# Kernel optimization log

Measured on AMD Instinct MI355X. Metric: run time of the kernel, lower is better.

The kernel has to match this reference:

```python
import jax, jax.numpy as jnp
import numpy as np

# Model hyperparameters (from init_kwargs)
B, C, H, W = 4, 3, 224, 224
P = 16            # patch size
E = 768           # embed_dim
NH = 12           # num_heads
DH = E // NH      # head dim
L = 2             # num_layers
DFF = 4 * E
OUT = 1000
NP_ = (H // P) * (W // P)   # 196 patches
ALPHA, BETA, GAMMA = 0.5, 0.5, 1.0
EPS = 1e-8
LN_EPS = 1e-5


def _layernorm(x, w, b):
    mu = x.mean(-1, keepdims=True)
    var = ((x - mu) ** 2).mean(-1, keepdims=True)
    return (x - mu) * jax.lax.rsqrt(var + LN_EPS) * w + b


def _tversky_attn(x, ln_w, ln_b, w_qkv, b_qkv, w_o, b_o):
    # x: [B,S,E]
    h = _layernorm(x, ln_w, ln_b)
    qkv = h @ w_qkv + b_qkv                       # [B,S,3E]
    q, k, v = jnp.split(qkv, 3, axis=-1)
    def heads(t):
        return t.reshape(t.shape[0], t.shape[1], NH, DH).transpose(0, 2, 1, 3)  # [B,NH,S,DH]
    q, k, v = heads(q), heads(k), heads(v)
    # Tversky similarity on non-negative feature memberships
    qp = jax.nn.relu(q)
    kp = jax.nn.relu(k)
    qs = qp.sum(-1)                               # [B,NH,S]
    ks = kp.sum(-1)                               # [B,NH,S]
    # pairwise L1: sum_d |q_i - k_j|   (dominant intermediate [B,NH,S,S,DH])
    l1 = jnp.abs(qp[:, :, :, None, :] - kp[:, :, None, :, :]).sum(-1)  # [B,NH,S,S]
    qsum = qs[:, :, :, None]
    ksum = ks[:, :, None, :]
    inter = 0.5 * (qsum + ksum - l1)              # sum min(q,k)
    a_minus_b = 0.5 * (l1 + qsum - ksum)          # sum relu(q-k)
    b_minus_a = 0.5 * (l1 - qsum + ksum)          # sum relu(k-q)
    scores = GAMMA * inter / (inter + ALPHA * a_minus_b + BETA * b_minus_a + EPS)
    attn = jax.nn.softmax(scores, axis=-1)        # [B,NH,S,S]
    o = jnp.einsum('bhij,bhjd->bhid', attn, v)    # [B,NH,S,DH]
    o = o.transpose(0, 2, 1, 3).reshape(x.shape[0], x.shape[1], E)
    return o @ w_o + b_o


def _forward(x, conv_w, conv_b, pos_embed, cls_token,
             ln1_w, ln1_b, attn_w, attn_b, proj_w, proj_b,
             ln2_w, ln2_b, fc1_w, fc1_b, fc2_w, fc2_b,
             lnf_w, lnf_b, head_w, head_b):
    b = x.shape[0]
    # patch embed: stride==kernel conv == non-overlapping patch projection
    xp = x.reshape(b, C, H // P, P, W // P, P)
    tok = jnp.einsum('bchpwq,ecpq->bhwe', xp, conv_w).reshape(b, NP_, E) + conv_b
    tok = tok + pos_embed                         # [B,196,E]
    cls = jnp.broadcast_to(cls_token, (b, 1, E))
    h = jnp.concatenate([cls, tok], axis=1)       # [B,197,E]
    for i in range(L):
        h = h + _tversky_attn(h, ln1_w[i], ln1_b[i], attn_w[i], attn_b[i], proj_w[i], proj_b[i])
        m = _layernorm(h, ln2_w[i], ln2_b[i])
        m = jax.nn.gelu(m @ fc1_w[i] + fc1_b[i])
        h = h + m @ fc2_w[i] + fc2_b[i]
    h = _layernorm(h, lnf_w, lnf_b)
    return h[:, 0] @ head_w + head_b              # [B,OUT]


def setup_inputs() -> dict:
    key = jax.random.key(0)
    ks = jax.random.split(key, 24)
    n = lambda k, shp, s=0.02: jax.random.normal(k, shp, dtype=jnp.float32) * s
    return {
        'x': jax.random.normal(ks[0], (B, C, H, W), dtype=jnp.float32),
        'conv_w': n(ks[1], (E, C, P, P)),
        'conv_b': jnp.zeros((E,), jnp.float32),
        'pos_embed': n(ks[2], (1, NP_, E)),
        'cls_token': n(ks[3], (1, 1, E)),
        'ln1_w': jnp.ones((L, E), jnp.float32),
        'ln1_b': jnp.zeros((L, E), jnp.float32),
        'attn_w': n(ks[4], (L, E, 3 * E)),
        'attn_b': jnp.zeros((L, 3 * E), jnp.float32),
        'proj_w': n(ks[5], (L, E, E)),
        'proj_b': jnp.zeros((L, E), jnp.float32),
        'ln2_w': jnp.ones((L, E), jnp.float32),
        'ln2_b': jnp.zeros((L, E), jnp.float32),
        'fc1_w': n(ks[6], (L, E, DFF)),
        'fc1_b': jnp.zeros((L, DFF), jnp.float32),
        'fc2_w': n(ks[7], (L, DFF, E)),
        'fc2_b': jnp.zeros((L, E), jnp.float32),
        'lnf_w': jnp.ones((E,), jnp.float32),
        'lnf_b': jnp.zeros((E,), jnp.float32),
        'head_w': n(ks[8], (E, OUT)),
        'head_b': jnp.zeros((OUT,), jnp.float32),
    }


def reference(x, conv_w, conv_b, pos_embed, cls_token,
              ln1_w, ln1_b, attn_w, attn_b, proj_w, proj_b,
              ln2_w, ln2_b, fc1_w, fc1_b, fc2_w, fc2_b,
              lnf_w, lnf_b, head_w, head_b):
    return _forward(x, conv_w, conv_b, pos_embed, cls_token,
                    ln1_w, ln1_b, attn_w, attn_b, proj_w, proj_b,
                    ln2_w, ln2_b, fc1_w, fc1_b, fc2_w, fc2_b,
                    lnf_w, lnf_b, head_w, head_b)
```

## Files before the change

### kernel.cpp

```cpp
#include <hip/hip_runtime.h>
#include <hip/hip_bf16.h>
#include <math.h>

#define B_  4
#define E_  768
#define NH_ 12
#define DH_ 64
#define DFF_ 3072
#define OUT_ 1000
#define S_  197
#define ROWS_ 788
#define QH_P 12608
#define KGP  16384

typedef __bf16 bf16x8_t __attribute__((ext_vector_type(8)));
typedef float f32x4_t __attribute__((ext_vector_type(4)));
typedef _Float16 f16x2_t __attribute__((ext_vector_type(2)));

#define HAS_FDOT2 __has_builtin(__builtin_amdgcn_fdot2)

__device__ __forceinline__ float gelu_f(float x) {
    float x3 = x * x * x;
    return 0.5f * x * (1.0f + tanhf(0.7978845608028654f * (x + 0.044715f * x3)));
}
__device__ __forceinline__ ushort f_to_bf16bits(float f) {
    __hip_bfloat16 b = __float2bfloat16(f);
    return *(ushort*)&b;
}
__device__ __forceinline__ ushort f_to_f16bits(float f) {
    _Float16 h = (_Float16)f;
    return __builtin_bit_cast(ushort, h);
}
__device__ __forceinline__ f16x2_t u2h(uint u) { return __builtin_bit_cast(f16x2_t, u); }
__device__ __forceinline__ f16x2_t min2(f16x2_t a, f16x2_t b) {
    return __builtin_elementwise_min(a, b);
}

#define WT_CONV   0
#define WT_LBASE  589824
#define WT_LSTRIDE 7077888
#define WT_QKV    0
#define WT_PROJ   1769472
#define WT_FC1    2359296
#define WT_FC2    4718592
__global__ __launch_bounds__(256) void prep_all_kernel(const float* __restrict__ x,
                                                       __hip_bfloat16* __restrict__ aim,
                                                       const float* __restrict__ attn_w,
                                                       const float* __restrict__ proj_w,
                                                       const float* __restrict__ fc1_w,
                                                       const float* __restrict__ fc2_w,
                                                       const float* __restrict__ conv_w,
                                                       __hip_bfloat16* __restrict__ wt) {
    int bid = blockIdx.x;
    if (bid < 588) {
        int id = bid * 256 + threadIdx.x;
        int row = id / 192, k4 = (id - row * 192) * 4;
        int b = row / 196, pr = row - b * 196;
        int hp = pr / 14, wp = pr - hp * 14;
        int c = k4 >> 8, rem = k4 & 255, p = rem >> 4, q = rem & 15;
        float4 v = *(const float4*)&x[(((size_t)(b * 3 + c) * 224) + hp * 16 + p) * 224 + wp * 16 + q];
        ushort4 o = make_ushort4(f_to_bf16bits(v.x), f_to_bf16bits(v.y), f_to_bf16bits(v.z), f_to_bf16bits(v.w));
        *(ushort4*)((ushort*)aim + (size_t)row * 768 + k4) = o;
        return;
    }
    int id = bid - 588;
    if (id >= 13824) {
        int off = ((id - 13824) * 256 + threadIdx.x) * 4;
        float4 v = *(const float4*)&conv_w[off];
        ushort4 o = make_ushort4(f_to_bf16bits(v.x), f_to_bf16bits(v.y), f_to_bf16bits(v.z), f_to_bf16bits(v.w));
        *(ushort4*)((ushort*)wt + WT_CONV + off) = o;
        return;
    }
    int l = id / 6912, r = id - l * 6912;
    const float* src;
    __hip_bfloat16* dst;
    int K, N, tile;
    size_t lbase = WT_LBASE + (size_t)l * WT_LSTRIDE;
    if (r < 1728)      { src = attn_w + (size_t)l * E_ * 3 * E_; dst = wt + lbase + WT_QKV;  K = E_;   N = 3 * E_; tile = r; }
    else if (r < 2304) { src = proj_w + (size_t)l * E_ * E_;     dst = wt + lbase + WT_PROJ; K = E_;   N = E_;     tile = r - 1728; }
    else if (r < 4608) { src = fc1_w + (size_t)l * E_ * DFF_;    dst = wt + lbase + WT_FC1;  K = E_;   N = DFF_;   tile = r - 2304; }
    else               { src = fc2_w + (size_t)l * DFF_ * E_;    dst = wt + lbase + WT_FC2;  K = DFF_; N = E_;     tile = r - 4608; }
    int ntn = N / 32;
    int kb = (tile / ntn) * 32, nb = (tile % ntn) * 32;
    __shared__ __hip_bfloat16 t[32][33];
    int tx = threadIdx.x & 31, ty = threadIdx.x >> 5;
#pragma unroll
    for (int rr = 0; rr < 32; rr += 8)
        t[ty + rr][tx] = __float2bfloat16(src[(size_t)(kb + ty + rr) * N + nb + tx]);
    __syncthreads();
#pragma unroll
    for (int rr = 0; rr < 32; rr += 8)
        dst[(size_t)(nb + ty + rr) * K + kb + tx] = t[tx][ty + rr];
}

#define BK 64
#define AP 72
__global__ __launch_bounds__(256) void gemm_mfma_kernel(const __hip_bfloat16* __restrict__ A,
                                                        const __hip_bfloat16* __restrict__ WT,
                                                        const float* __restrict__ bias,
                                                        const float* __restrict__ res,
                                                        float* __restrict__ Cf,
                                                        __hip_bfloat16* __restrict__ Cb,
                                                        float* __restrict__ partbase,
                                                        int M, int N, int K, int act, int KS,
                                                        int res_pitch) {
    __shared__ __align__(16) ushort Asb[2][64 * AP];
    __shared__ __align__(16) ushort Bsb[2][64 * AP];
    const int tid = threadIdx.x;
    const int wave = tid >> 6, lane = tid & 63;
    const int quad = lane >> 4, l15 = lane & 15;
    const int wm = wave >> 1, wn = wave & 1;
    const int m0 = blockIdx.y * 64, n0 = blockIdx.x * 64;

    const int Kc   = K / KS;
    const int kbeg = blockIdx.z * Kc;
    const int n_it = Kc / BK;

    f32x4_t acc[2][2] = {};

    const int c0r = tid >> 3,         c0o = (tid & 7) * 8;
    const int c1r = (tid + 256) >> 3, c1o = c0o;

    uint4 pa0, pa1, pb0, pb1;
    auto load_tile = [&](int kk) {
        pa0 = make_uint4(0, 0, 0, 0);
        pa1 = pa0;
        int gm = m0 + c0r;
        if (gm < M) pa0 = *(const uint4*)&A[(size_t)gm * K + kk + c0o];
        gm = m0 + c1r;
        if (gm < M) pa1 = *(const uint4*)&A[(size_t)gm * K + kk + c1o];
        pb0 = *(const uint4*)&WT[(size_t)(n0 + c0r) * K + kk + c0o];
        pb1 = *(const uint4*)&WT[(size_t)(n0 + c1r) * K + kk + c1o];
    };
    auto store_tile = [&](int buf) {
        *(uint4*)&Asb[buf][c0r * AP + c0o] = pa0;
        *(uint4*)&Asb[buf][c1r * AP + c1o] = pa1;
        *(uint4*)&Bsb[buf][c0r * AP + c0o] = pb0;
        *(uint4*)&Bsb[buf][c1r * AP + c1o] = pb1;
    };

    load_tile(kbeg);
    store_tile(0);
    if (n_it > 1) load_tile(kbeg + BK);
    __syncthreads();

    for (int it = 0; it < n_it; ++it) {
        const int cur = it & 1, nxt = cur ^ 1;
        if (it + 1 < n_it) {
            store_tile(nxt);
            if (it + 2 < n_it) load_tile(kbeg + (it + 2) * BK);
        }
        const ushort* As = Asb[cur];
        const ushort* Bs = Bsb[cur];
#pragma unroll
        for (int ks = 0; ks < BK; ks += 32) {
            bf16x8_t a0 = *(const bf16x8_t*)&As[(32 * wm + l15) * AP + ks + 8 * quad];
            bf16x8_t a1 = *(const bf16x8_t*)&As[(32 * wm + 16 + l15) * AP + ks + 8 * quad];
            bf16x8_t b0 = *(const bf16x8_t*)&Bs[(32 * wn + l15) * AP + ks + 8 * quad];
            bf16x8_t b1 = *(const bf16x8_t*)&Bs[(32 * wn + 16 + l15) * AP + ks + 8 * quad];
            acc[0][0] = __builtin_amdgcn_mfma_f32_16x16x32_bf16(a0, b0, acc[0][0], 0, 0, 0);
            acc[0][1] = __builtin_amdgcn_mfma_f32_16x16x32_bf16(a0, b1, acc[0][1], 0, 0, 0);
            acc[1][0] = __builtin_amdgcn_mfma_f32_16x16x32_bf16(a1, b0, acc[1][0], 0, 0, 0);
            acc[1][1] = __builtin_amdgcn_mfma_f32_16x16x32_bf16(a1, b1, acc[1][1], 0, 0, 0);
        }
        __syncthreads();
    }

    if (partbase) {
        float* P = partbase + (size_t)blockIdx.z * M * N;
#pragma unroll
        for (int mi = 0; mi < 2; ++mi)
#pragma unroll
            for (int ni = 0; ni < 2; ++ni) {
                int gn = n0 + 32 * wn + 16 * ni + l15;
#pragma unroll
                for (int r = 0; r < 4; ++r) {
                    int gm = m0 + 32 * wm + 16 * mi + quad * 4 + r;
                    if (gm < M) P[(size_t)gm * N + gn] = acc[mi][ni][r];
                }
            }
        return;
    }

#pragma unroll
    for (int mi = 0; mi < 2; ++mi)
#pragma unroll
        for (int ni = 0; ni < 2; ++ni) {
            int gn = n0 + 32 * wn + 16 * ni + l15;
#pragma unroll
            for (int r = 0; r < 4; ++r) {
                int gm = m0 + 32 * wm + 16 * mi + quad * 4 + r;
                if (gm < M) {
                    float v = acc[mi][ni][r] + bias[gn];
                    if (act == 1) v = gelu_f(v);
                    if (res) v += res[(size_t)gm * res_pitch + gn];
                    if (Cf) Cf[(size_t)gm * N + gn] = v;
                    else    Cb[(size_t)gm * N + gn] = __float2bfloat16(v);
                }
            }
        }
}

__global__ __launch_bounds__(256) void embed_ln_kernel(const float* __restrict__ p0,
                                                       const float* __restrict__ p1,
                                                       const float* __restrict__ cb,
                                                       const float* __restrict__ pe,
                                                       const float* __restrict__ ct,
                                                       const float* __restrict__ lw,
                                                       const float* __restrict__ lb,
                                                       float* __restrict__ h,
                                                       __hip_bfloat16* __restrict__ y) {
    int row = blockIdx.x, tid = threadIdx.x;
    int b = row / S_, s = row - b * S_;
    float v[3];
#pragma unroll
    for (int c = 0; c < 3; ++c) {
        int e = tid + c * 256;
        float t;
        if (s == 0) t = ct[e];
        else {
            int pr = s - 1;
            size_t gi = (size_t)(b * 196 + pr) * E_ + e;
            t = p0[gi] + p1[gi] + cb[e] + pe[(size_t)pr * E_ + e];
        }
        h[(size_t)row * E_ + e] = t;
        v[c] = t;
    }
    float sm = v[0] + v[1] + v[2];
    float sq = v[0] * v[0] + v[1] * v[1] + v[2] * v[2];
#pragma unroll
    for (int m = 1; m < 64; m <<= 1) {
        sm += __shfl_xor(sm, m, 64);
        sq += __shfl_xor(sq, m, 64);
    }
    __shared__ float ss[4], sqs[4];
    int wave = tid >> 6, lane = tid & 63;
    if (lane == 0) { ss[wave] = sm; sqs[wave] = sq; }
    __syncthreads();
    sm = ss[0] + ss[1] + ss[2] + ss[3];
    sq = sqs[0] + sqs[1] + sqs[2] + sqs[3];
    float mu   = sm * (1.0f / 768.0f);
    float var  = sq * (1.0f / 768.0f) - mu * mu;
    float rstd = rsqrtf(var + 1e-5f);
    __hip_bfloat16* yr = y + (size_t)row * E_;
#pragma unroll
    for (int c = 0; c < 3; ++c) {
        int e = tid + c * 256;
        yr[e] = __float2bfloat16((v[c] - mu) * rstd * lw[e] + lb[e]);
    }
}

__global__ __launch_bounds__(256) void layernorm_kernel(const float* __restrict__ x,
                                                        const float* __restrict__ w,
                                                        const float* __restrict__ b,
                                                        __hip_bfloat16* __restrict__ y) {
    int row = blockIdx.x;
    const float* xr = x + (size_t)row * E_;
    int tid = threadIdx.x;
    float v0 = xr[tid], v1 = xr[tid + 256], v2 = xr[tid + 512];
    float s  = v0 + v1 + v2;
    float sq = v0 * v0 + v1 * v1 + v2 * v2;
#pragma unroll
    for (int m = 1; m < 64; m <<= 1) {
        s  += __shfl_xor(s, m, 64);
        sq += __shfl_xor(sq, m, 64);
    }
    __shared__ float ss[4], sqs[4];
    int wave = tid >> 6, lane = tid & 63;
    if (lane == 0) { ss[wave] = s; sqs[wave] = sq; }
    __syncthreads();
    s  = ss[0] + ss[1] + ss[2] + ss[3];
    sq = sqs[0] + sqs[1] + sqs[2] + sqs[3];
    float mu   = s * (1.0f / 768.0f);
    float var  = sq * (1.0f / 768.0f) - mu * mu;
    float rstd = rsqrtf(var + 1e-5f);
    __hip_bfloat16* yr = y + (size_t)row * E_;
    yr[tid]       = __float2bfloat16((v0 - mu) * rstd * w[tid]       + b[tid]);
    yr[tid + 256] = __float2bfloat16((v1 - mu) * rstd * w[tid + 256] + b[tid + 256]);
    yr[tid + 512] = __float2bfloat16((v2 - mu) * rstd * w[tid + 512] + b[tid + 512]);
}

__global__ __launch_bounds__(256) void reduce_ln_kernel(const float* __restrict__ p0,
                                                        const float* __restrict__ p1,
                                                        const float* __restrict__ bias,
                                                        float* __restrict__ h,
                                                        const float* __restrict__ lw,
                                                        const float* __restrict__ lb,
                                                        __hip_bfloat16* __restrict__ y) {
    int row = blockIdx.x, tid = threadIdx.x;
    float v[3];
#pragma unroll
    for (int c = 0; c < 3; ++c) {
        int e = tid + c * 256;
        size_t gi = (size_t)row * E_ + e;
        float t = bias[e] + p0[gi] + p1[gi] + h[gi];
        h[gi] = t;
        v[c] = t;
    }
    float s  = v[0] + v[1] + v[2];
    float sq = v[0] * v[0] + v[1] * v[1] + v[2] * v[2];
#pragma unroll
    for (int m = 1; m < 64; m <<= 1) {
        s  += __shfl_xor(s, m, 64);
        sq += __shfl_xor(sq, m, 64);
    }
    __shared__ float ss[4], sqs[4];
    int wave = tid >> 6, lane = tid & 63;
    if (lane == 0) { ss[wave] = s; sqs[wave] = sq; }
    __syncthreads();
    s  = ss[0] + ss[1] + ss[2] + ss[3];
    sq = sqs[0] + sqs[1] + sqs[2] + sqs[3];
    float mu   = s * (1.0f / 768.0f);
    float var  = sq * (1.0f / 768.0f) - mu * mu;
    float rstd = rsqrtf(var + 1e-5f);
    __hip_bfloat16* yr = y + (size_t)row * E_;
#pragma unroll
    for (int c = 0; c < 3; ++c) {
        int e = tid + c * 256;
        yr[e] = __float2bfloat16((v[c] - mu) * rstd * lw[e] + lb[e]);
    }
}

__global__ __launch_bounds__(256) void attn_prep_kernel(const float* __restrict__ p0,
                                                        const float* __restrict__ p1,
                                                        const float* __restrict__ ab,
                                                        ushort* __restrict__ kg,
                                                        float* __restrict__ ksg,
                                                        ushort* __restrict__ qg,
                                                        ushort* __restrict__ vgt,
                                                        float* __restrict__ qsg,
                                                        int nrows) {
    const int tid = threadIdx.x, lane = tid & 63, wv = tid >> 6;
    const int hh = blockIdx.x, bb = blockIdx.y, z = blockIdx.z;
    const int head = bb * NH_ + hh;
    if (z < 2) {
        const int jb = z * 128;
        float* ksrow = ksg + (size_t)head * 256;
        for (int c = 0; c < 32; ++c) {
            int j = jb + c * 4 + wv;
            float val;
            if (j < S_) {
                size_t g = ((size_t)(bb * S_ + j)) * (3 * E_) + E_ + hh * DH_ + lane;
                val = fmaxf(p0[g] + p1[g] + ab[E_ + hh * DH_ + lane], 0.f);
            } else val = -64.f;
            kg[(size_t)head * KGP + j * 64 + lane] = f_to_f16bits(val);
            float s = (j < S_) ? val : 0.f;
#pragma unroll
            for (int m = 1; m < 64; m <<= 1) s += __shfl_xor(s, m, 64);
            if (lane == 0) ksrow[j] = s;
        }
    } else if (z < 4) {
        __shared__ ushort t[64][130];
        const int jb = (z - 2) * 128;
        for (int c = 0; c < 32; ++c) {
            int idx = c * 256 + tid;
            int jl = idx >> 6, d = idx & 63;
            int j = jb + jl;
            float val = 0.f;
            if (j < S_) {
                size_t g = ((size_t)(bb * S_ + j)) * (3 * E_) + 2 * E_ + hh * DH_ + d;
                val = p0[g] + p1[g] + ab[2 * E_ + hh * DH_ + d];
            }
            t[d][jl] = f_to_bf16bits(val);
        }
        __syncthreads();
        for (int c = 0; c < 32; ++c) {
            int idx = c * 256 + tid;
            int d = idx >> 7, jl = idx & 127;
            vgt[(size_t)head * KGP + d * 256 + jb + jl] = t[d][jl];
        }
    } else {
        const int ib = (z - 4) * 128;
        float* qsrow = qsg + (size_t)head * 200;
        for (int c = 0; c < 32; ++c) {
            int i = ib + c * 4 + wv;
            if (i >= nrows) continue;
            size_t g = ((size_t)(bb * S_ + i)) * (3 * E_) + hh * DH_ + lane;
            float val = fmaxf(p0[g] + p1[g] + ab[hh * DH_ + lane], 0.f);
            qg[(size_t)head * QH_P + i * 64 + lane] = f_to_f16bits(val);
            float s = val;
#pragma unroll
            for (int m = 1; m < 64; m <<= 1) s += __shfl_xor(s, m, 64);
            if (lane == 0) qsrow[i] = s;
        }
    }
}

__global__ __launch_bounds__(256) void tversky_attn_kernel(const ushort* __restrict__ qg,
                                                           const ushort* __restrict__ kg,
                                                           const float* __restrict__ ksg,
                                                           const ushort* __restrict__ vgt,
                                                           const float* __restrict__ qsg,
                                                           __hip_bfloat16* __restrict__ ao,
                                                           int nrows) {
    __shared__ __align__(16) ushort kf[16384];
    __shared__ __align__(16) float ks_l[256];
    __shared__ __align__(16) ushort q_l[1024];
    __shared__ __align__(16) ushort p_l[4096];
    __shared__ __align__(16) float den_l[16];

    const int tid = threadIdx.x, wv = tid >> 6, lane = tid & 63;
    const int quad = lane >> 4, l15 = lane & 15;
    const int ch = blockIdx.x, hh = blockIdx.y, bb = blockIdx.z;
    const int head = bb * NH_ + hh;

    {
        const ushort* kgh = kg + (size_t)head * KGP;
#pragma unroll
        for (int g = 0; g < 8; ++g) {
            int idx = g * 256 + tid;
            int row = idx >> 3, c = idx & 7;
            int sw = c ^ ((row >> 1) & 7);
            *(uint4*)&kf[row * 64 + sw * 8] = *(const uint4*)&kgh[idx * 8];
        }
        ks_l[tid] = ksg[(size_t)head * 256 + tid];
    }
    const int i0 = ch * 16 + wv * 4;
    if (lane < 32) {
        int r = lane >> 3, c = lane & 7;
        int i = i0 + r;
        uint4 qv = make_uint4(0, 0, 0, 0);
        if (i < nrows) qv = *(const uint4*)&qg[(size_t)head * QH_P + i * 64 + c * 8];
        *(uint4*)&q_l[wv * 256 + r * 64 + c * 8] = qv;
    }
    float qs_r[4];
#pragma unroll
    for (int r = 0; r < 4; ++r)
        qs_r[r] = (i0 + r < nrows) ? qsg[(size_t)head * 200 + i0 + r] : 0.f;
    __syncthreads();

#if HAS_FDOT2
    const f16x2_t one2 = __builtin_bit_cast(f16x2_t, 0x3C003C00u);
#endif
    float den_r[4] = {0.f, 0.f, 0.f, 0.f};
#pragma unroll
    for (int ph = 0; ph < 2; ++ph) {
        const int jb = ph * 128;
        uint4 kreg0[8], kreg1[8];
        const int r0 = (jb + 2 * lane) * 64;
#pragma unroll
        for (int c = 0; c < 8; ++c) {
            int sw = (c ^ (lane & 7)) * 8;
            kreg0[c] = *(const uint4*)&kf[r0 + sw];
            kreg1[c] = *(const uint4*)&kf[r0 + 64 + sw];
        }
        float acc0[4] = {0.f, 0.f, 0.f, 0.f};
        float acc1[4] = {0.f, 0.f, 0.f, 0.f};
#pragma unroll
        for (int c = 0; c < 8; ++c) {
            uint k0p[4] = {kreg0[c].x, kreg0[c].y, kreg0[c].z, kreg0[c].w};
            uint k1p[4] = {kreg1[c].x, kreg1[c].y, kreg1[c].z, kreg1[c].w};
#pragma unroll
            for (int r = 0; r < 4; ++r) {
                uint4 qu = *(const uint4*)&q_l[wv * 256 + r * 64 + c * 8];
                uint qp[4] = {qu.x, qu.y, qu.z, qu.w};
#if HAS_FDOT2
#pragma unroll
                for (int p = 0; p < 4; ++p) {
                    f16x2_t qq = u2h(qp[p]);
                    acc0[r] = __builtin_amdgcn_fdot2(min2(qq, u2h(k0p[p])), one2, acc0[r], false);
                    acc1[r] = __builtin_amdgcn_fdot2(min2(qq, u2h(k1p[p])), one2, acc1[r], false);
                }
#else
                f16x2_t m0 = min2(u2h(qp[0]), u2h(k0p[0]));
                f16x2_t m1 = min2(u2h(qp[0]), u2h(k1p[0]));
#pragma unroll
                for (int p = 1; p < 4; ++p) {
                    m0 = m0 + min2(u2h(qp[p]), u2h(k0p[p]));
                    m1 = m1 + min2(u2h(qp[p]), u2h(k1p[p]));
                }
                acc0[r] += (float)m0[0] + (float)m0[1];
                acc1[r] += (float)m1[0] + (float)m1[1];
#endif
            }
        }
        float2 ks2 = *(const float2*)&ks_l[jb + 2 * lane];
#pragma unroll
        for (int r = 0; r < 4; ++r) {
            float s0 = qs_r[r] + ks2.x, s1 = qs_r[r] + ks2.y;
            float e0 = __expf((2.f * acc0[r]) / (s0 + 2e-8f));
            float e1 = __expf((2.f * acc1[r]) / (s1 + 2e-8f));
            float sum = e0 + e1;
#pragma unroll
            for (int m = 1; m < 64; m <<= 1) sum += __shfl_xor(sum, m, 64);
            den_r[r] += sum;
            uint pw = (uint)f_to_bf16bits(e0) | ((uint)f_to_bf16bits(e1) << 16);
            int i = wv * 4 + r;
            *(uint*)&p_l[(i * 256 + jb + 2 * lane) ^ ((i & 7) * 8)] = pw;
        }
    }
    if (lane == 0) {
#pragma unroll
        for (int r = 0; r < 4; ++r) den_l[wv * 4 + r] = den_r[r];
    }
    __syncthreads();

    const ushort* vb = vgt + (size_t)head * KGP + (size_t)(16 * wv + l15) * 256;
    f32x4_t accv = {0.f, 0.f, 0.f, 0.f};
#pragma unroll
    for (int st = 0; st < 8; ++st) {
        bf16x8_t a = *(const bf16x8_t*)&p_l[(l15 * 256 + st * 32 + quad * 8) ^ ((l15 & 7) * 8)];
        bf16x8_t b = *(const bf16x8_t*)&vb[st * 32 + quad * 8];
        accv = __builtin_amdgcn_mfma_f32_16x16x32_bf16(a, b, accv, 0, 0, 0);
    }
    float4 dv = *(const float4*)&den_l[quad * 4];
    float dar[4] = {dv.x, dv.y, dv.z, dv.w};
#pragma unroll
    for (int t = 0; t < 4; ++t) {
        int ig = ch * 16 + quad * 4 + t;
        if (ig < nrows)
            ao[((size_t)(bb * nrows + ig)) * E_ + hh * DH_ + 16 * wv + l15] =
                __float2bfloat16(accv[t] / dar[t]);
    }
}

__global__ __launch_bounds__(256) void head_ln_kernel(const float* __restrict__ hc,
                                                      const float* __restrict__ pc0,
                                                      const float* __restrict__ pc1,
                                                      const float* __restrict__ fb,
                                                      const float* __restrict__ lw,
                                                      const float* __restrict__ lb,
                                                      const float* __restrict__ hw,
                                                      const float* __restrict__ hb,
                                                      float* __restrict__ out) {
    int b = blockIdx.y;
    int tid = threadIdx.x;
    const float* xr0 = hc  + (size_t)b * E_;
    const float* pr0 = pc0 + (size_t)b * E_;
    const float* pr1 = pc1 + (size_t)b * E_;
    float v0 = xr0[tid]       + pr0[tid]       + pr1[tid]       + fb[tid];
    float v1 = xr0[tid + 256] + pr0[tid + 256] + pr1[tid + 256] + fb[tid + 256];
    float v2 = xr0[tid + 512] + pr0[tid + 512] + pr1[tid + 512] + fb[tid + 512];
    float s  = v0 + v1 + v2;
    float sq = v0 * v0 + v1 * v1 + v2 * v2;
#pragma unroll
    for (int m = 1; m < 64; m <<= 1) {
        s  += __shfl_xor(s, m, 64);
        sq += __shfl_xor(sq, m, 64);
    }
    __shared__ float ss[4], sqs[4];
    __shared__ float xr[E_];
    __shared__ float partial[4][64];
    int wave = tid >> 6, lane = tid & 63;
    if (lane == 0) { ss[wave] = s; sqs[wave] = sq; }
    __syncthreads();
    s  = ss[0] + ss[1] + ss[2] + ss[3];
    sq = sqs[0] + sqs[1] + sqs[2] + sqs[3];
    float mu   = s * (1.0f / 768.0f);
    float var  = sq * (1.0f / 768.0f) - mu * mu;
    float rstd = rsqrtf(var + 1e-5f);
    xr[tid]       = (v0 - mu) * rstd * lw[tid]       + lb[tid];
    xr[tid + 256] = (v1 - mu) * rstd * lw[tid + 256] + lb[tid + 256];
    xr[tid + 512] = (v2 - mu) * rstd * lw[tid + 512] + lb[tid + 512];
    __syncthreads();
    int nl = tid & 63, eq = tid >> 6;
    int n = blockIdx.x * 64 + nl;
    float acc = 0.f;
    if (n < OUT_) {
        int e0 = eq * 192;
        for (int e = e0; e < e0 + 192; ++e) acc += xr[e] * hw[(size_t)e * OUT_ + n];
    }
    partial[eq][nl] = acc;
    __syncthreads();
    if (eq == 0 && n < OUT_)
        out[(size_t)b * OUT_ + n] = partial[0][nl] + partial[1][nl] + partial[2][nl] + partial[3][nl] + hb[n];
}

extern "C" void kernel_launch(void* const* d_in, const int* in_sizes, int n_in,
                              void* d_out, int out_size, void* d_ws, size_t ws_size,
                              hipStream_t stream) {
    const float* x        = (const float*)d_in[0];
    const float* conv_w   = (const float*)d_in[1];
    const float* conv_b   = (const float*)d_in[2];
    const float* pos_e    = (const float*)d_in[3];
    const float* cls_t    = (const float*)d_in[4];
    const float* ln1_w    = (const float*)d_in[5];
    const float* ln1_b    = (const float*)d_in[6];
    const float* attn_w   = (const float*)d_in[7];
    const float* attn_b   = (const float*)d_in[8];
    const float* proj_w   = (const float*)d_in[9];
    const float* proj_b   = (const float*)d_in[10];
    const float* ln2_w    = (const float*)d_in[11];
    const float* ln2_b    = (const float*)d_in[12];
    const float* fc1_w    = (const float*)d_in[13];
    const float* fc1_b    = (const float*)d_in[14];
    const float* fc2_w    = (const float*)d_in[15];
    const float* fc2_b    = (const float*)d_in[16];
    const float* lnf_w    = (const float*)d_in[17];
    const float* lnf_b    = (const float*)d_in[18];
    const float* head_w   = (const float*)d_in[19];
    const float* head_b   = (const float*)d_in[20];
    float* out = (float*)d_out;

    float* h       = (float*)d_ws;
    float* part0q  = h + 605184;
    float* part1q  = part0q + 1815552;
    float* part    = part1q + 1815552;
    float* hc      = part + 1210368;
    float* partc   = hc + 3072;
    float* ksg     = partc + 6144;
    float* qsg     = ksg + 12288;
    __hip_bfloat16* lnb  = (__hip_bfloat16*)(qsg + 9600);
    __hip_bfloat16* ao   = lnb + 605184;
    __hip_bfloat16* hid  = ao + 605184;
    __hip_bfloat16* aim  = hid + 2420736;
    __hip_bfloat16* wt   = aim + 602112;
    ushort* kg  = (ushort*)(wt + 14745600);
    ushort* vgt = kg + 786432;
    ushort* qg  = vgt + 786432;
    __hip_bfloat16* lnb4 = (__hip_bfloat16*)(qg + 605184);
    __hip_bfloat16* hid4 = lnb4 + 3072;

    prep_all_kernel<<<14988, 256, 0, stream>>>(x, aim, attn_w, proj_w, fc1_w, fc2_w, conv_w, wt);
    {
        dim3 grid(E_ / 64, 13, 2);
        gemm_mfma_kernel<<<grid, 256, 0, stream>>>(aim, wt + WT_CONV, nullptr, nullptr, nullptr,
                                                   nullptr, part, 784, E_, E_, 0, 2, 0);
    }
    embed_ln_kernel<<<ROWS_, 256, 0, stream>>>(part, part + 602112, conv_b,
                                               pos_e, cls_t, ln1_w, ln1_b, h, lnb);

    {
        const __hip_bfloat16* wl = wt + WT_LBASE;
        {
            dim3 grid((3 * E_) / 64, 13, 2);
            gemm_mfma_kernel<<<grid, 256, 0, stream>>>(lnb, wl + WT_QKV, nullptr, nullptr,
                                                       nullptr, nullptr, part0q,
                                                       ROWS_, 3 * E_, E_, 0, 2, 0);
        }
        attn_prep_kernel<<<dim3(NH_, B_, 6), 256, 0, stream>>>(
            part0q, part1q, attn_b, kg, ksg, qg, vgt, qsg, S_);
        tversky_attn_kernel<<<dim3(13, NH_, B_), 256, 0, stream>>>(
            qg, kg, ksg, vgt, qsg, ao, S_);
        {
            dim3 grid(E_ / 64, 13, 2);
            gemm_mfma_kernel<<<grid, 256, 0, stream>>>(ao, wl + WT_PROJ, nullptr, nullptr, nullptr,
                                                       nullptr, part, ROWS_, E_, E_, 0, 2, 0);
        }
        reduce_ln_kernel<<<ROWS_, 256, 0, stream>>>(part, part + 605184, proj_b,
                                                    h, ln2_w, ln2_b, lnb);
        {
            dim3 grid(DFF_ / 64, 13);
            gemm_mfma_kernel<<<grid, 256, 0, stream>>>(lnb, wl + WT_FC1, fc1_b,
                                                       nullptr, nullptr, hid, nullptr,
                                                       ROWS_, DFF_, E_, 1, 1, 0);
        }
        {
            dim3 grid(E_ / 64, 13, 2);
            gemm_mfma_kernel<<<grid, 256, 0, stream>>>(hid, wl + WT_FC2, nullptr, nullptr, nullptr,
                                                       nullptr, part, ROWS_, E_, DFF_, 0, 2, 0);
        }
        reduce_ln_kernel<<<ROWS_, 256, 0, stream>>>(part, part + 605184, fc2_b,
                                                    h, ln1_w + E_, ln1_b + E_, lnb);
    }

    {
        const __hip_bfloat16* wl = wt + WT_LBASE + WT_LSTRIDE;
        {
            dim3 grid((3 * E_) / 64, 13, 2);
            gemm_mfma_kernel<<<grid, 256, 0, stream>>>(lnb, wl + WT_QKV, nullptr, nullptr,
                                                       nullptr, nullptr, part0q,
                                                       ROWS_, 3 * E_, E_, 0, 2, 0);
        }
        attn_prep_kernel<<<dim3(NH_, B_, 6), 256, 0, stream>>>(
            part0q, part1q, attn_b + 3 * E_, kg, ksg, qg, vgt, qsg, 1);
        tversky_attn_kernel<<<dim3(1, NH_, B_), 256, 0, stream>>>(
            qg, kg, ksg, vgt, qsg, ao, 1);
        {
            dim3 grid(E_ / 64, 1, 1);
            gemm_mfma_kernel<<<grid, 256, 0, stream>>>(ao, wl + WT_PROJ, proj_b + E_, h,
                                                       hc, nullptr, nullptr,
                                                       4, E_, E_, 0, 1, S_ * E_);
        }
        layernorm_kernel<<<4, 256, 0, stream>>>(hc, ln2_w + E_, ln2_b + E_, lnb4);
        {
            dim3 grid(DFF_ / 64, 1, 1);
            gemm_mfma_kernel<<<grid, 256, 0, stream>>>(lnb4, wl + WT_FC1, fc1_b + DFF_,
                                                       nullptr, nullptr, hid4, nullptr,
                                                       4, DFF_, E_, 1, 1, 0);
        }
        {
            dim3 grid(E_ / 64, 1, 2);
            gemm_mfma_kernel<<<grid, 256, 0, stream>>>(hid4, wl + WT_FC2, nullptr, nullptr, nullptr,
                                                       nullptr, partc, 4, E_, DFF_, 0, 2, 0);
        }
    }

    {
        dim3 grid((OUT_ + 63) / 64, B_);
        head_ln_kernel<<<grid, 256, 0, stream>>>(hc, partc, partc + 3072, fc2_b + E_,
                                                 lnf_w, lnf_b, head_w, head_b, out);
    }
}
```

Before: 344.3 us.

## Add 128x128-tile MFMA GEMM for QKV/FC1/FC2 and vectorize weight transpose

Adds a 128x128-tile bf16 MFMA GEMM kernel with BK=32 and uses it for the QKV, FC1 and FC2 projections, with FC2 split-K raised to 6. reduce_ln now sums a variable number of partials, and the partial buffer is enlarged to hold them. The weight transpose in prep moves to 64x64 tiles using float4 register transposes instead of shared memory, which cuts the block count. Larger tiles give more data reuse per block, but with only 788 rows the grids are smaller, so fewer CUs may be kept busy. The extra split-K partials also add memory traffic.

```diff
diff --git a/kernel.cpp b/kernel.cpp
--- a/kernel.cpp
+++ b/kernel.cpp
@@ -64,33 +64,37 @@
         return;
     }
     int id = bid - 588;
-    if (id >= 13824) {
-        int off = ((id - 13824) * 256 + threadIdx.x) * 4;
+    if (id < 3456) {
+        int l = id / 1728, r = id - l * 1728;
+        const float* src;
+        __hip_bfloat16* dst;
+        int K, N, tile;
+        size_t lbase = WT_LBASE + (size_t)l * WT_LSTRIDE;
+        if (r < 432)       { src = attn_w + (size_t)l * E_ * 3 * E_; dst = wt + lbase + WT_QKV;  K = E_;   N = 3 * E_; tile = r; }
+        else if (r < 576)  { src = proj_w + (size_t)l * E_ * E_;     dst = wt + lbase + WT_PROJ; K = E_;   N = E_;     tile = r - 432; }
+        else if (r < 1152) { src = fc1_w + (size_t)l * E_ * DFF_;    dst = wt + lbase + WT_FC1;  K = E_;   N = DFF_;   tile = r - 576; }
+        else               { src = fc2_w + (size_t)l * DFF_ * E_;    dst = wt + lbase + WT_FC2;  K = DFF_; N = E_;     tile = r - 1152; }
+        int ntn = N >> 6;
+        int kb = (tile / ntn) * 64, nb = (tile % ntn) * 64;
+        int kq = (threadIdx.x & 15) * 4, nq = (threadIdx.x >> 4) * 4;
+        const float* s0 = src + (size_t)(kb + kq) * N + nb + nq;
+        float4 v0 = *(const float4*)(s0);
+        float4 v1 = *(const float4*)(s0 + N);
+        float4 v2 = *(const float4*)(s0 + 2 * N);
+        float4 v3 = *(const float4*)(s0 + 3 * N);
+        __hip_bfloat16* d0 = dst + (size_t)(nb + nq) * K + kb + kq;
+        *(ushort4*)(d0)         = make_ushort4(f_to_bf16bits(v0.x), f_to_bf16bits(v1.x), f_to_bf16bits(v2.x), f_to_bf16bits(v3.x));
+        *(ushort4*)(d0 + K)     = make_ushort4(f_to_bf16bits(v0.y), f_to_bf16bits(v1.y), f_to_bf16bits(v2.y), f_to_bf16bits(v3.y));
+        *(ushort4*)(d0 + 2 * K) = make_ushort4(f_to_bf16bits(v0.z), f_to_bf16bits(v1.z), f_to_bf16bits(v2.z), f_to_bf16bits(v3.z));
+        *(ushort4*)(d0 + 3 * K) = make_ushort4(f_to_bf16bits(v0.w), f_to_bf16bits(v1.w), f_to_bf16bits(v2.w), f_to_bf16bits(v3.w));
+        return;
+    }
+    {
+        int off = ((id - 3456) * 256 + threadIdx.x) * 4;
         float4 v = *(const float4*)&conv_w[off];
         ushort4 o = make_ushort4(f_to_bf16bits(v.x), f_to_bf16bits(v.y), f_to_bf16bits(v.z), f_to_bf16bits(v.w));
         *(ushort4*)((ushort*)wt + WT_CONV + off) = o;
-        return;
-    }
-    int l = id / 6912, r = id - l * 6912;
-    const float* src;
-    __hip_bfloat16* dst;
-    int K, N, tile;
-    size_t lbase = WT_LBASE + (size_t)l * WT_LSTRIDE;
-    if (r < 1728)      { src = attn_w + (size_t)l * E_ * 3 * E_; dst = wt + lbase + WT_QKV;  K = E_;   N = 3 * E_; tile = r; }
-    else if (r < 2304) { src = proj_w + (size_t)l * E_ * E_;     dst = wt + lbase + WT_PROJ; K = E_;   N = E_;     tile = r - 1728; }
-    else if (r < 4608) { src = fc1_w + (size_t)l * E_ * DFF_;    dst = wt + lbase + WT_FC1;  K = E_;   N = DFF_;   tile = r - 2304; }
-    else               { src = fc2_w + (size_t)l * DFF_ * E_;    dst = wt + lbase + WT_FC2;  K = DFF_; N = E_;     tile = r - 4608; }
-    int ntn = N / 32;
-    int kb = (tile / ntn) * 32, nb = (tile % ntn) * 32;
-    __shared__ __hip_bfloat16 t[32][33];
-    int tx = threadIdx.x & 31, ty = threadIdx.x >> 5;
-#pragma unroll
-    for (int rr = 0; rr < 32; rr += 8)
-        t[ty + rr][tx] = __float2bfloat16(src[(size_t)(kb + ty + rr) * N + nb + tx]);
-    __syncthreads();
-#pragma unroll
-    for (int rr = 0; rr < 32; rr += 8)
-        dst[(size_t)(nb + ty + rr) * K + kb + tx] = t[tx][ty + rr];
+    }
 }
 
 #define BK 64
@@ -201,6 +205,111 @@
         }
 }
 
+#define BK2 32
+#define AP2 40
+__global__ __launch_bounds__(256) void gemm_mfma128_kernel(const __hip_bfloat16* __restrict__ A,
+                                                           const __hip_bfloat16* __restrict__ WT,
+                                                           const float* __restrict__ bias,
+                                                           float* __restrict__ Cf,
+                                                           __hip_bfloat16* __restrict__ Cb,
+                                                           float* __restrict__ partbase,
+                                                           int M, int N, int K, int act, int KS) {
+    __shared__ __align__(16) ushort Asb[2][128 * AP2];
+    __shared__ __align__(16) ushort Bsb[2][128 * AP2];
+    const int tid = threadIdx.x;
+    const int wave = tid >> 6, lane = tid & 63;
+    const int quad = lane >> 4, l15 = lane & 15;
+    const int wm = wave >> 1, wn = wave & 1;
+    const int m0 = blockIdx.y * 128, n0 = blockIdx.x * 128;
+
+    const int Kc   = K / KS;
+    const int kbeg = blockIdx.z * Kc;
+    const int n_it = Kc / BK2;
+
+    f32x4_t acc[4][4] = {};
+
+    const int sr = tid >> 2, sc = (tid & 3) * 8;
+
+    uint4 pa0, pa1, pb0, pb1;
+    auto load_tile = [&](int kk) {
+        pa0 = make_uint4(0, 0, 0, 0);
+        pa1 = pa0;
+        int gm = m0 + sr;
+        if (gm < M) pa0 = *(const uint4*)&A[(size_t)gm * K + kk + sc];
+        gm = m0 + sr + 64;
+        if (gm < M) pa1 = *(const uint4*)&A[(size_t)gm * K + kk + sc];
+        pb0 = *(const uint4*)&WT[(size_t)(n0 + sr) * K + kk + sc];
+        pb1 = *(const uint4*)&WT[(size_t)(n0 + sr + 64) * K + kk + sc];
+    };
+    auto store_tile = [&](int buf) {
+        *(uint4*)&Asb[buf][sr * AP2 + sc]        = pa0;
+        *(uint4*)&Asb[buf][(sr + 64) * AP2 + sc] = pa1;
+        *(uint4*)&Bsb[buf][sr * AP2 + sc]        = pb0;
+        *(uint4*)&Bsb[buf][(sr + 64) * AP2 + sc] = pb1;
+    };
+
+    load_tile(kbeg);
+    store_tile(0);
+    if (n_it > 1) load_tile(kbeg + BK2);
+    __syncthreads();
+
+    for (int it = 0; it < n_it; ++it) {
+        const int cur = it & 1, nxt = cur ^ 1;
+        if (it + 1 < n_it) {
+            store_tile(nxt);
+            if (it + 2 < n_it) load_tile(kbeg + (it + 2) * BK2);
+        }
+        const ushort* As = Asb[cur];
+        const ushort* Bs = Bsb[cur];
+        bf16x8_t af[4], bf[4];
+#pragma unroll
+        for (int mi = 0; mi < 4; ++mi)
+            af[mi] = *(const bf16x8_t*)&As[(64 * wm + 16 * mi + l15) * AP2 + 8 * quad];
+#pragma unroll
+        for (int ni = 0; ni < 4; ++ni)
+            bf[ni] = *(const bf16x8_t*)&Bs[(64 * wn + 16 * ni + l15) * AP2 + 8 * quad];
+#pragma unroll
+        for (int mi = 0; mi < 4; ++mi)
+#pragma unroll
+            for (int ni = 0; ni < 4; ++ni)
+                acc[mi][ni] = __builtin_amdgcn_mfma_f32_16x16x32_bf16(af[mi], bf[ni], acc[mi][ni], 0, 0, 0);
+        __syncthreads();
+    }
+
+    if (partbase) {
+        float* P = partbase + (size_t)blockIdx.z * M * N;
+#pragma unroll
+        for (int mi = 0; mi < 4; ++mi)
+#pragma unroll
+            for (int ni = 0; ni < 4; ++ni) {
+                int gn = n0 + 64 * wn + 16 * ni + l15;
+#pragma unroll
+                for (int r = 0; r < 4; ++r) {
+                    int gm = m0 + 64 * wm + 16 * mi + quad * 4 + r;
+                    if (gm < M) P[(size_t)gm * N + gn] = acc[mi][ni][r];
+                }
+            }
+        return;
+    }
+
+#pragma unroll
+    for (int mi = 0; mi < 4; ++mi)
+#pragma unroll
+        for (int ni = 0; ni < 4; ++ni) {
+            int gn = n0 + 64 * wn + 16 * ni + l15;
+#pragma unroll
+            for (int r = 0; r < 4; ++r) {
+                int gm = m0 + 64 * wm + 16 * mi + quad * 4 + r;
+                if (gm < M) {
+                    float v = acc[mi][ni][r] + bias[gn];
+                    if (act == 1) v = gelu_f(v);
+                    if (Cf) Cf[(size_t)gm * N + gn] = v;
+                    else    Cb[(size_t)gm * N + gn] = __float2bfloat16(v);
+                }
+            }
+        }
+}
+
 __global__ __launch_bounds__(256) void embed_ln_kernel(const float* __restrict__ p0,
                                                        const float* __restrict__ p1,
                                                        const float* __restrict__ cb,
@@ -280,8 +389,8 @@
     yr[tid + 512] = __float2bfloat16((v2 - mu) * rstd * w[tid + 512] + b[tid + 512]);
 }
 
-__global__ __launch_bounds__(256) void reduce_ln_kernel(const float* __restrict__ p0,
-                                                        const float* __restrict__ p1,
+__global__ __launch_bounds__(256) void reduce_ln_kernel(const float* __restrict__ parts,
+                                                        int np, size_t pstride,
                                                         const float* __restrict__ bias,
                                                         float* __restrict__ h,
                                                         const float* __restrict__ lw,
@@ -293,7 +402,8 @@
     for (int c = 0; c < 3; ++c) {
         int e = tid + c * 256;
         size_t gi = (size_t)row * E_ + e;
-        float t = bias[e] + p0[gi] + p1[gi] + h[gi];
+        float t = bias[e] + h[gi];
+        for (int z = 0; z < np; ++z) t += parts[z * pstride + gi];
         h[gi] = t;
         v[c] = t;
     }
@@ -596,7 +706,7 @@
     float* part0q  = h + 605184;
     float* part1q  = part0q + 1815552;
     float* part    = part1q + 1815552;
-    float* hc      = part + 1210368;
+    float* hc      = part + 3631104;
     float* partc   = hc + 3072;
     float* ksg     = partc + 6144;
     float* qsg     = ksg + 12288;
@@ -611,7 +721,7 @@
     __hip_bfloat16* lnb4 = (__hip_bfloat16*)(qg + 605184);
     __hip_bfloat16* hid4 = lnb4 + 3072;
 
-    prep_all_kernel<<<14988, 256, 0, stream>>>(x, aim, attn_w, proj_w, fc1_w, fc2_w, conv_w, wt);
+    prep_all_kernel<<<4620, 256, 0, stream>>>(x, aim, attn_w, proj_w, fc1_w, fc2_w, conv_w, wt);
     {
         dim3 grid(E_ / 64, 13, 2);
         gemm_mfma_kernel<<<grid, 256, 0, stream>>>(aim, wt + WT_CONV, nullptr, nullptr, nullptr,
@@ -623,10 +733,10 @@
     {
         const __hip_bfloat16* wl = wt + WT_LBASE;
         {
-            dim3 grid((3 * E_) / 64, 13, 2);
-            gemm_mfma_kernel<<<grid, 256, 0, stream>>>(lnb, wl + WT_QKV, nullptr, nullptr,
-                                                       nullptr, nullptr, part0q,
-                                                       ROWS_, 3 * E_, E_, 0, 2, 0);
+            dim3 grid((3 * E_) / 128, 7, 2);
+            gemm_mfma128_kernel<<<grid, 256, 0, stream>>>(lnb, wl + WT_QKV, nullptr,
+                                                          nullptr, nullptr, part0q,
+                                                          ROWS_, 3 * E_, E_, 0, 2);
         }
         attn_prep_kernel<<<dim3(NH_, B_, 6), 256, 0, stream>>>(
             part0q, part1q, attn_b, kg, ksg, qg, vgt, qsg, S_);
@@ -637,30 +747,31 @@
             gemm_mfma_kernel<<<grid, 256, 0, stream>>>(ao, wl + WT_PROJ, nullptr, nullptr, nullptr,
                                                        nullptr, part, ROWS_, E_, E_, 0, 2, 0);
         }
-        reduce_ln_kernel<<<ROWS_, 256, 0, stream>>>(part, part + 605184, proj_b,
+        reduce_ln_kernel<<<ROWS_, 256, 0, stream>>>(part, 2, 605184, proj_b,
                                                     h, ln2_w, ln2_b, lnb);
         {
-            dim3 grid(DFF_ / 64, 13);
-            gemm_mfma_kernel<<<grid, 256, 0, stream>>>(lnb, wl + WT_FC1, fc1_b,
-                                                       nullptr, nullptr, hid, nullptr,
-                                                       ROWS_, DFF_, E_, 1, 1, 0);
+            dim3 grid(DFF_ / 128, 7);
+            gemm_mfma128_kernel<<<grid, 256, 0, stream>>>(lnb, wl + WT_FC1, fc1_b,
+                                                          nullptr, hid, nullptr,
+                                                          ROWS_, DFF_, E_, 1, 1);
         }
         {
-            dim3 grid(E_ / 64, 13, 2);
-            gemm_mfma_kernel<<<grid, 256, 0, stream>>>(hid, wl + WT_FC2, nullptr, nullptr, nullptr,
-                                                       nullptr, part, ROWS_, E_, DFF_, 0, 2, 0);
-        }
-        reduce_ln_kernel<<<ROWS_, 256, 0, stream>>>(part, part + 605184, fc2_b,
+            dim3 grid(E_ / 128, 7, 6);
+            gemm_mfma128_kernel<<<grid, 256, 0, stream>>>(hid, wl + WT_FC2, nullptr,
+                                                          nullptr, nullptr, part,
+                                                          ROWS_, E_, DFF_, 0, 6);
+        }
+        reduce_ln_kernel<<<ROWS_, 256, 0, stream>>>(part, 6, 605184, fc2_b,
                                                     h, ln1_w + E_, ln1_b + E_, lnb);
     }
 
     {
         const __hip_bfloat16* wl = wt + WT_LBASE + WT_LSTRIDE;
         {
-            dim3 grid((3 * E_) / 64, 13, 2);
-            gemm_mfma_kernel<<<grid, 256, 0, stream>>>(lnb, wl + WT_QKV, nullptr, nullptr,
-                                                       nullptr, nullptr, part0q,
-                                                       ROWS_, 3 * E_, E_, 0, 2, 0);
+            dim3 grid((3 * E_) / 128, 7, 2);
+            gemm_mfma128_kernel<<<grid, 256, 0, stream>>>(lnb, wl + WT_QKV, nullptr,
+                                                          nullptr, nullptr, part0q,
+                                                          ROWS_, 3 * E_, E_, 0, 2);
         }
         attn_prep_kernel<<<dim3(NH_, B_, 6), 256, 0, stream>>>(
             part0q, part1q, attn_b + 3 * E_, kg, ksg, qg, vgt, qsg, 1);
```

New measurement: 372.0 us. 8.0% more time.

## Vectorize weight transpose prep and skip full-sequence Q projection in last layer

Applied to the files above, without the earlier changes.

Rewrites the weight transpose/convert prep to use 64x64 tiles with float4 loads and ushort4 register-transposed stores, dropping the shared-memory staging and cutting the block count. In the last layer only the CLS query is needed, so the QKV GEMM now computes just the K and V columns (written at an offset into the partial buffer), and the CLS query row is computed directly in attn_prep from the raw fp32 weights. reduce_ln is generalized to take a variable number of partials. The direct per-head query dot product uses strided fp32 weight reads, which may be inefficient but is small.

```diff
diff --git a/kernel.cpp b/kernel.cpp
--- a/kernel.cpp
+++ b/kernel.cpp
@@ -64,33 +64,37 @@
         return;
     }
     int id = bid - 588;
-    if (id >= 13824) {
-        int off = ((id - 13824) * 256 + threadIdx.x) * 4;
+    if (id < 3456) {
+        int l = id / 1728, r = id - l * 1728;
+        const float* src;
+        __hip_bfloat16* dst;
+        int K, N, tile;
+        size_t lbase = WT_LBASE + (size_t)l * WT_LSTRIDE;
+        if (r < 432)       { src = attn_w + (size_t)l * E_ * 3 * E_; dst = wt + lbase + WT_QKV;  K = E_;   N = 3 * E_; tile = r; }
+        else if (r < 576)  { src = proj_w + (size_t)l * E_ * E_;     dst = wt + lbase + WT_PROJ; K = E_;   N = E_;     tile = r - 432; }
+        else if (r < 1152) { src = fc1_w + (size_t)l * E_ * DFF_;    dst = wt + lbase + WT_FC1;  K = E_;   N = DFF_;   tile = r - 576; }
+        else               { src = fc2_w + (size_t)l * DFF_ * E_;    dst = wt + lbase + WT_FC2;  K = DFF_; N = E_;     tile = r - 1152; }
+        int ntn = N >> 6;
+        int kb = (tile / ntn) * 64, nb = (tile % ntn) * 64;
+        int kq = (threadIdx.x & 15) * 4, nq = (threadIdx.x >> 4) * 4;
+        const float* s0 = src + (size_t)(kb + kq) * N + nb + nq;
+        float4 v0 = *(const float4*)(s0);
+        float4 v1 = *(const float4*)(s0 + N);
+        float4 v2 = *(const float4*)(s0 + 2 * N);
+        float4 v3 = *(const float4*)(s0 + 3 * N);
+        __hip_bfloat16* d0 = dst + (size_t)(nb + nq) * K + kb + kq;
+        *(ushort4*)(d0)         = make_ushort4(f_to_bf16bits(v0.x), f_to_bf16bits(v1.x), f_to_bf16bits(v2.x), f_to_bf16bits(v3.x));
+        *(ushort4*)(d0 + K)     = make_ushort4(f_to_bf16bits(v0.y), f_to_bf16bits(v1.y), f_to_bf16bits(v2.y), f_to_bf16bits(v3.y));
+        *(ushort4*)(d0 + 2 * K) = make_ushort4(f_to_bf16bits(v0.z), f_to_bf16bits(v1.z), f_to_bf16bits(v2.z), f_to_bf16bits(v3.z));
+        *(ushort4*)(d0 + 3 * K) = make_ushort4(f_to_bf16bits(v0.w), f_to_bf16bits(v1.w), f_to_bf16bits(v2.w), f_to_bf16bits(v3.w));
+        return;
+    }
+    {
+        int off = ((id - 3456) * 256 + threadIdx.x) * 4;
         float4 v = *(const float4*)&conv_w[off];
         ushort4 o = make_ushort4(f_to_bf16bits(v.x), f_to_bf16bits(v.y), f_to_bf16bits(v.z), f_to_bf16bits(v.w));
         *(ushort4*)((ushort*)wt + WT_CONV + off) = o;
-        return;
-    }
-    int l = id / 6912, r = id - l * 6912;
-    const float* src;
-    __hip_bfloat16* dst;
-    int K, N, tile;
-    size_t lbase = WT_LBASE + (size_t)l * WT_LSTRIDE;
-    if (r < 1728)      { src = attn_w + (size_t)l * E_ * 3 * E_; dst = wt + lbase + WT_QKV;  K = E_;   N = 3 * E_; tile = r; }
-    else if (r < 2304) { src = proj_w + (size_t)l * E_ * E_;     dst = wt + lbase + WT_PROJ; K = E_;   N = E_;     tile = r - 1728; }
-    else if (r < 4608) { src = fc1_w + (size_t)l * E_ * DFF_;    dst = wt + lbase + WT_FC1;  K = E_;   N = DFF_;   tile = r - 2304; }
-    else               { src = fc2_w + (size_t)l * DFF_ * E_;    dst = wt + lbase + WT_FC2;  K = DFF_; N = E_;     tile = r - 4608; }
-    int ntn = N / 32;
-    int kb = (tile / ntn) * 32, nb = (tile % ntn) * 32;
-    __shared__ __hip_bfloat16 t[32][33];
-    int tx = threadIdx.x & 31, ty = threadIdx.x >> 5;
-#pragma unroll
-    for (int rr = 0; rr < 32; rr += 8)
-        t[ty + rr][tx] = __float2bfloat16(src[(size_t)(kb + ty + rr) * N + nb + tx]);
-    __syncthreads();
-#pragma unroll
-    for (int rr = 0; rr < 32; rr += 8)
-        dst[(size_t)(nb + ty + rr) * K + kb + tx] = t[tx][ty + rr];
+    }
 }
 
 #define BK 64
@@ -103,7 +107,7 @@
                                                         __hip_bfloat16* __restrict__ Cb,
                                                         float* __restrict__ partbase,
                                                         int M, int N, int K, int act, int KS,
-                                                        int res_pitch) {
+                                                        int res_pitch, int pn, int nofs) {
     __shared__ __align__(16) ushort Asb[2][64 * AP];
     __shared__ __align__(16) ushort Bsb[2][64 * AP];
     const int tid = threadIdx.x;
@@ -167,7 +171,7 @@
     }
 
     if (partbase) {
-        float* P = partbase + (size_t)blockIdx.z * M * N;
+        float* P = partbase + (size_t)blockIdx.z * M * pn;
 #pragma unroll
         for (int mi = 0; mi < 2; ++mi)
 #pragma unroll
@@ -176,7 +180,7 @@
 #pragma unroll
                 for (int r = 0; r < 4; ++r) {
                     int gm = m0 + 32 * wm + 16 * mi + quad * 4 + r;
-                    if (gm < M) P[(size_t)gm * N + gn] = acc[mi][ni][r];
+                    if (gm < M) P[(size_t)gm * pn + nofs + gn] = acc[mi][ni][r];
                 }
             }
         return;
@@ -280,8 +284,8 @@
     yr[tid + 512] = __float2bfloat16((v2 - mu) * rstd * w[tid + 512] + b[tid + 512]);
 }
 
-__global__ __launch_bounds__(256) void reduce_ln_kernel(const float* __restrict__ p0,
-                                                        const float* __restrict__ p1,
+__global__ __launch_bounds__(256) void reduce_ln_kernel(const float* __restrict__ parts,
+                                                        int np, size_t pstride,
                                                         const float* __restrict__ bias,
                                                         float* __restrict__ h,
                                                         const float* __restrict__ lw,
@@ -293,7 +297,8 @@
     for (int c = 0; c < 3; ++c) {
         int e = tid + c * 256;
         size_t gi = (size_t)row * E_ + e;
-        float t = bias[e] + p0[gi] + p1[gi] + h[gi];
+        float t = bias[e] + h[gi];
+        for (int z = 0; z < np; ++z) t += parts[z * pstride + gi];
         h[gi] = t;
         v[c] = t;
     }
@@ -329,7 +334,9 @@
                                                         ushort* __restrict__ qg,
                                                         ushort* __restrict__ vgt,
                                                         float* __restrict__ qsg,
-                                                        int nrows) {
+                                                        int nrows,
+                                                        const __hip_bfloat16* __restrict__ xin,
+                                                        const float* __restrict__ wraw) {
     const int tid = threadIdx.x, lane = tid & 63, wv = tid >> 6;
     const int hh = blockIdx.x, bb = blockIdx.y, z = blockIdx.z;
     const int head = bb * NH_ + hh;
@@ -370,6 +377,29 @@
             vgt[(size_t)head * KGP + d * 256 + jb + jl] = t[d][jl];
         }
     } else {
+        if (nrows == 1) {
+            if (z == 5) return;
+            __shared__ float sacc[4][64];
+            const __hip_bfloat16* xr = xin + (size_t)(bb * S_) * E_;
+            const float* wcol = wraw + hh * DH_;
+            float acc = 0.f;
+            const int k0 = wv * 192;
+#pragma unroll 4
+            for (int k = k0; k < k0 + 192; ++k)
+                acc += __bfloat162float(xr[k]) * wcol[(size_t)k * (3 * E_) + lane];
+            sacc[wv][lane] = acc;
+            __syncthreads();
+            if (tid < 64) {
+                float q = sacc[0][tid] + sacc[1][tid] + sacc[2][tid] + sacc[3][tid] + ab[hh * DH_ + tid];
+                q = fmaxf(q, 0.f);
+                qg[(size_t)head * QH_P + tid] = f_to_f16bits(q);
+                float s = q;
+#pragma unroll
+                for (int m = 1; m < 64; m <<= 1) s += __shfl_xor(s, m, 64);
+                if (tid == 0) qsg[(size_t)head * 200] = s;
+            }
+            return;
+        }
         const int ib = (z - 4) * 128;
         float* qsrow = qsg + (size_t)head * 200;
         for (int c = 0; c < 32; ++c) {
@@ -596,7 +626,7 @@
     float* part0q  = h + 605184;
     float* part1q  = part0q + 1815552;
     float* part    = part1q + 1815552;
-    float* hc      = part + 1210368;
+    float* hc      = part + 3631104;
     float* partc   = hc + 3072;
     float* ksg     = partc + 6144;
     float* qsg     = ksg + 12288;
@@ -611,11 +641,11 @@
     __hip_bfloat16* lnb4 = (__hip_bfloat16*)(qg + 605184);
     __hip_bfloat16* hid4 = lnb4 + 3072;
 
-    prep_all_kernel<<<14988, 256, 0, stream>>>(x, aim, attn_w, proj_w, fc1_w, fc2_w, conv_w, wt);
+    prep_all_kernel<<<4620, 256, 0, stream>>>(x, aim, attn_w, proj_w, fc1_w, fc2_w, conv_w, wt);
     {
         dim3 grid(E_ / 64, 13, 2);
         gemm_mfma_kernel<<<grid, 256, 0, stream>>>(aim, wt + WT_CONV, nullptr, nullptr, nullptr,
-                                                   nullptr, part, 784, E_, E_, 0, 2, 0);
+                                                   nullptr, part, 784, E_, E_, 0, 2, 0, E_, 0);
     }
     embed_ln_kernel<<<ROWS_, 256, 0, stream>>>(part, part + 602112, conv_b,
                                                pos_e, cls_t, ln1_w, ln1_b, h, lnb);
@@ -626,63 +656,64 @@
             dim3 grid((3 * E_) / 64, 13, 2);
             gemm_mfma_kernel<<<grid, 256, 0, stream>>>(lnb, wl + WT_QKV, nullptr, nullptr,
                                                        nullptr, nullptr, part0q,
-                                                       ROWS_, 3 * E_, E_, 0, 2, 0);
+                                                       ROWS_, 3 * E_, E_, 0, 2, 0, 3 * E_, 0);
         }
         attn_prep_kernel<<<dim3(NH_, B_, 6), 256, 0, stream>>>(
-            part0q, part1q, attn_b, kg, ksg, qg, vgt, qsg, S_);
+            part0q, part1q, attn_b, kg, ksg, qg, vgt, qsg, S_, lnb, attn_w);
         tversky_attn_kernel<<<dim3(13, NH_, B_), 256, 0, stream>>>(
             qg, kg, ksg, vgt, qsg, ao, S_);
         {
             dim3 grid(E_ / 64, 13, 2);
             gemm_mfma_kernel<<<grid, 256, 0, stream>>>(ao, wl + WT_PROJ, nullptr, nullptr, nullptr,
-                                                       nullptr, part, ROWS_, E_, E_, 0, 2, 0);
-        }
-        reduce_ln_kernel<<<ROWS_, 256, 0, stream>>>(part, part + 605184, proj_b,
+                                                       nullptr, part, ROWS_, E_, E_, 0, 2, 0, E_, 0);
+        }
+        reduce_ln_kernel<<<ROWS_, 256, 0, stream>>>(part, 2, 605184, proj_b,
                                                     h, ln2_w, ln2_b, lnb);
         {
             dim3 grid(DFF_ / 64, 13);
             gemm_mfma_kernel<<<grid, 256, 0, stream>>>(lnb, wl + WT_FC1, fc1_b,
                                                        nullptr, nullptr, hid, nullptr,
-                                                       ROWS_, DFF_, E_, 1, 1, 0);
+                                                       ROWS_, DFF_, E_, 1, 1, 0, DFF_, 0);
         }
         {
             dim3 grid(E_ / 64, 13, 2);
             gemm_mfma_kernel<<<grid, 256, 0, stream>>>(hid, wl + WT_FC2, nullptr, nullptr, nullptr,
-                                                       nullptr, part, ROWS_, E_, DFF_, 0, 2, 0);
-        }
-        reduce_ln_kernel<<<ROWS_, 256, 0, stream>>>(part, part + 605184, fc2_b,
+                                                       nullptr, part, ROWS_, E_, DFF_, 0, 2, 0, E_, 0);
+        }
+        reduce_ln_kernel<<<ROWS_, 256, 0, stream>>>(part, 2, 605184, fc2_b,
                                                     h, ln1_w + E_, ln1_b + E_, lnb);
     }
 
     {
         const __hip_bfloat16* wl = wt + WT_LBASE + WT_LSTRIDE;
         {
-            dim3 grid((3 * E_) / 64, 13, 2);
-            gemm_mfma_kernel<<<grid, 256, 0, stream>>>(lnb, wl + WT_QKV, nullptr, nullptr,
+            dim3 grid(1536 / 64, 13, 2);
+            gemm_mfma_kernel<<<grid, 256, 0, stream>>>(lnb, wl + WT_QKV + 768 * E_, nullptr, nullptr,
                                                        nullptr, nullptr, part0q,
-                                                       ROWS_, 3 * E_, E_, 0, 2, 0);
+                                                       ROWS_, 1536, E_, 0, 2, 0, 3 * E_, 768);
         }
         attn_prep_kernel<<<dim3(NH_, B_, 6), 256, 0, stream>>>(
-            part0q, part1q, attn_b + 3 * E_, kg, ksg, qg, vgt, qsg, 1);
+            part0q, part1q, attn_b + 3 * E_, kg, ksg, qg, vgt, qsg, 1,
+            lnb, attn_w + (size_t)E_ * 3 * E_);
         tversky_attn_kernel<<<dim3(1, NH_, B_), 256, 0, stream>>>(
             qg, kg, ksg, vgt, qsg, ao, 1);
         {
             dim3 grid(E_ / 64, 1, 1);
             gemm_mfma_kernel<<<grid, 256, 0, stream>>>(ao, wl + WT_PROJ, proj_b + E_, h,
                                                        hc, nullptr, nullptr,
-                                                       4, E_, E_, 0, 1, S_ * E_);
+                                                       4, E_, E_, 0, 1, S_ * E_, E_, 0);
         }
         layernorm_kernel<<<4, 256, 0, stream>>>(hc, ln2_w + E_, ln2_b + E_, lnb4);
         {
             dim3 grid(DFF_ / 64, 1, 1);
             gemm_mfma_kernel<<<grid, 256, 0, stream>>>(lnb4, wl + WT_FC1, fc1_b + DFF_,
                                                        nullptr, nullptr, hid4, nullptr,
-                                                       4, DFF_, E_, 1, 1, 0);
+                                                       4, DFF_, E_, 1, 1, 0, DFF_, 0);
         }
         {
             dim3 grid(E_ / 64, 1, 2);
             gemm_mfma_kernel<<<grid, 256, 0, stream>>>(hid4, wl + WT_FC2, nullptr, nullptr, nullptr,
-                                                       nullptr, partc, 4, E_, DFF_, 0, 2, 0);
+                                                       nullptr, partc, 4, E_, DFF_, 0, 2, 0, E_, 0);
         }
     }
 
```

Result: no change. 342.0 us (-0.7%).
